# Kernel tuning notes

Measured on AMD Instinct MI355X. Metric: run time of the kernel, lower is better.

Reference implementation:

```python
import jax, jax.numpy as jnp
import numpy as np

B, D, E, H, T = 16384, 32, 8, 64, 10  # batch, state_dim, n_experts, hidden, time points
TEMP = 1.0  # gating temperature


def setup_inputs() -> dict:
    key = jax.random.key(0)
    ks = jax.random.split(key, 12)
    w = lambda k, shape, fan_in: (jax.random.normal(k, shape, jnp.float32) / np.sqrt(fan_in)).astype(jnp.float32)
    return {
        "x0": jax.random.normal(ks[0], (B, D), jnp.float32),
        "t_span": jnp.linspace(0.0, 1.0, T).astype(jnp.float32),
        # per-expert time-conditioned MLP: (x, t) -> H -> H -> D
        "W1": w(ks[1], (E, D + 1, H), D + 1), "b1": jnp.zeros((E, H), jnp.float32),
        "W2": w(ks[2], (E, H, H), H),          "b2": jnp.zeros((E, H), jnp.float32),
        "W3": w(ks[3], (E, H, D), H),          "b3": jnp.zeros((E, D), jnp.float32),
        # gating MLP on concat(x, dx_init): 2D -> H -> E
        "Gw1": w(ks[4], (2 * D, H), 2 * D), "Gb1": jnp.zeros((H,), jnp.float32),
        "Gw2": w(ks[5], (H, E), H),         "Gb2": jnp.zeros((E,), jnp.float32),
    }


def _dyn(t, x, W1, b1, W2, b2, W3, b3, Gw1, Gb1, Gw2, Gb2):
    # AME-ODE training-path dynamics: uniform-weighted init, gate, weighted sum
    inp = jnp.concatenate([x, jnp.ones((x.shape[0], 1), x.dtype) * t], axis=-1)  # [B, D+1]
    h = jnp.tanh(jnp.einsum('bi,eih->beh', inp, W1) + b1)
    h = jnp.tanh(jnp.einsum('beh,ehg->beg', h, W2) + b2)
    f = jnp.einsum('beg,egd->bed', h, W3) + b3          # all-expert dynamics [B, E, D]
    dx_init = f.mean(axis=1)                             # uniform weights 1/E
    g = jnp.tanh(jnp.concatenate([x, dx_init], -1) @ Gw1 + Gb1)
    wgt = jax.nn.softmax((g @ Gw2 + Gb2) / TEMP, axis=-1)  # [B, E]
    return jnp.einsum('be,bed->bd', wgt, f)


def reference(x0, t_span, W1, b1, W2, b2, W3, b3, Gw1, Gb1, Gw2, Gb2):
    params = (W1, b1, W2, b2, W3, b3, Gw1, Gb1, Gw2, Gb2)

    def step(x, ts):
        t0, t1 = ts[0], ts[1]
        dt = t1 - t0
        k1 = _dyn(t0, x, *params)
        k2 = _dyn(t0 + 0.5 * dt, x + 0.5 * dt * k1, *params)
        k3 = _dyn(t0 + 0.5 * dt, x + 0.5 * dt * k2, *params)
        k4 = _dyn(t1, x + dt * k3, *params)
        xn = x + (dt / 6.0) * (k1 + 2.0 * k2 + 2.0 * k3 + k4)
        return xn, xn

    pairs = jnp.stack([t_span[:-1], t_span[1:]], axis=1)  # [T-1, 2]
    _, traj = jax.lax.scan(step, x0, pairs)               # [T-1, B, D]
    traj = jnp.concatenate([x0[None], traj], axis=0)       # [T, B, D]
    return jnp.transpose(traj, (1, 0, 2))                  # [B, T, D]
```

## Files before the change

kernel.cpp:

```cpp
#include <hip/hip_runtime.h>
#include <hip/hip_bf16.h>

typedef unsigned int u32;
typedef unsigned short u16;
typedef __attribute__((ext_vector_type(8))) short short8;
typedef __attribute__((ext_vector_type(4))) float f32x4;
typedef __attribute__((ext_vector_type(4))) u32 u32x4;

#define DD 32
#define EE 8
#define HH 64
#define TT 10
#define BATCH 16384
#define EPB 32

__device__ __forceinline__ float fast_tanh(float x) {
  float e = __expf(2.f * x);
  return 1.f - 2.f * __builtin_amdgcn_rcpf(e + 1.f);
}
__device__ __forceinline__ u16 f2b_rn(float v) {
  return (u16)((__float_as_uint(v) + 0x8000u) >> 16);
}
__device__ __forceinline__ u32 pack2_rn(float a, float b) {
  return ((__float_as_uint(a) + 0x8000u) >> 16) |
         ((__float_as_uint(b) + 0x8000u) & 0xffff0000u);
}
__device__ __forceinline__ float unp_lo(u32 p) { return __uint_as_float(p << 16); }
__device__ __forceinline__ float unp_hi(u32 p) { return __uint_as_float(p & 0xffff0000u); }
__device__ __forceinline__ short8 lds_frag(const u32* p) {
  u32x4 w = *(const u32x4*)p;
  return __builtin_bit_cast(short8, w);
}

__global__ __launch_bounds__(512) void ame_ode_kernel(
    const float* __restrict__ x0, const float* __restrict__ tspan,
    const float* __restrict__ W1, const float* __restrict__ b1,
    const float* __restrict__ W2, const float* __restrict__ b2,
    const float* __restrict__ W3, const float* __restrict__ b3,
    const float* __restrict__ Gw1, const float* __restrict__ Gb1,
    const float* __restrict__ Gw2, const float* __restrict__ Gb2,
    float* __restrict__ out)
{
  __shared__ __align__(16) u32 xdb[EPB][36];
  __shared__ __align__(16) u32 fs[EPB][130];
  __shared__ __align__(16) float lg[EPB][9];
  __shared__ __align__(16) u32 hsbuf[EE * 16 * 36];
  __shared__ __align__(16) u16 gw1t[HH][72];
  __shared__ __align__(16) u16 gw2t[16][72];

  const int tid  = threadIdx.x;
  const int lane = tid & 63;
  const int l15  = lane & 15;
  const int quad = lane >> 4;
  const int e    = __builtin_amdgcn_readfirstlane(tid >> 6);
  const int elem = lane & 31;
  const int hf   = lane >> 5;
  const int cc   = 2 * e + hf;
  const int d0   = 2 * cc;
  const int bglob = blockIdx.x * EPB;

  const float* W1f = W1 + e * (DD + 1) * HH;
  const float* b1f = b1 + e * HH;
  const float* W2f = W2 + e * HH * HH;
  const float* b2f = b2 + e * HH;
  const float* W3f = W3 + e * HH * DD;
  const float* b3f = b3 + e * DD;

  short8 bw1[4], bw2[2][4], bw3[2][2];
  #pragma unroll
  for (int nt = 0; nt < 4; nt++)
    #pragma unroll
    for (int j = 0; j < 8; j++)
      bw1[nt][j] = (short)f2b_rn(W1f[(quad * 8 + j) * HH + nt * 16 + l15]);
  #pragma unroll
  for (int ks = 0; ks < 2; ks++)
    #pragma unroll
    for (int nt = 0; nt < 4; nt++)
      #pragma unroll
      for (int j = 0; j < 8; j++)
        bw2[ks][nt][j] = (short)f2b_rn(W2f[(ks * 32 + quad * 8 + j) * HH + nt * 16 + l15]);
  #pragma unroll
  for (int ks = 0; ks < 2; ks++)
    #pragma unroll
    for (int dt2 = 0; dt2 < 2; dt2++)
      #pragma unroll
      for (int j = 0; j < 8; j++)
        bw3[ks][dt2][j] = (short)f2b_rn(W3f[(ks * 32 + quad * 8 + j) * DD + dt2 * 16 + l15]);

  u32 c1p[4], c2p[2], c3p;
  #pragma unroll
  for (int nt = 0; nt < 4; nt++)
    c1p[nt] = pack2_rn(b1f[nt * 16 + l15], W1f[DD * HH + nt * 16 + l15]);
  #pragma unroll
  for (int p = 0; p < 2; p++)
    c2p[p] = pack2_rn(b2f[(2 * p) * 16 + l15], b2f[(2 * p + 1) * 16 + l15]);
  c3p = pack2_rn(b3f[l15], b3f[16 + l15]);
  const float gb1v = Gb1[(e >> 1) * 16 + l15];
  const float gb2v = (l15 < 8) ? Gb2[l15] : 0.f;

  for (int idx = tid; idx < HH * HH; idx += 512) {
    int h = idx >> 6, i = idx & 63;
    gw1t[h][i] = f2b_rn(Gw1[i * HH + h]);
  }
  for (int idx = tid; idx < 16 * HH; idx += 512) {
    int j = idx >> 6, h = idx & 63;
    gw2t[j][h] = (j < EE) ? f2b_rn(Gw2[h * EE + j]) : (u16)0;
  }

  float xst0, xst1, xac0, xac1;
  {
    const float2 v = *(const float2*)(x0 + (bglob + elem) * DD + d0);
    xst0 = v.x; xst1 = v.y; xac0 = v.x; xac1 = v.y;
    xdb[elem][cc] = pack2_rn(v.x, v.y);
    *(float2*)(out + ((bglob + elem) * TT) * DD + d0) = v;
  }
  __syncthreads();

  u32* const hw = hsbuf + e * 576;
  u16* const hw16 = (u16*)hw;
  u16* const fw16 = (u16*)&fs[0][0];
  const u32* const gw1t32 = (const u32*)&gw1t[0][0];
  const u32* const gw2t32 = (const u32*)&gw2t[0][0];
  const u16* const gs16 = (const u16*)hsbuf;
  u16* const gsw16 = (u16*)hsbuf;

  #pragma unroll 1
  for (int step = 0; step < TT - 1; step++) {
    const float t0 = tspan[step];
    const float t1 = tspan[step + 1];
    const float dt = t1 - t0;

    #pragma unroll 1
    for (int s = 0; s < 4; s++) {
      const float tcur = (s == 0) ? t0 : ((s == 3) ? t1 : t0 + 0.5f * dt);

      #pragma unroll
      for (int mt = 0; mt < 2; mt++) {
        const short8 a1 = lds_frag(&xdb[mt * 16 + l15][quad * 4]);
        f32x4 h1a[4];
        #pragma unroll
        for (int nt = 0; nt < 4; nt++) {
          const float iv = __builtin_fmaf(tcur, unp_hi(c1p[nt]), unp_lo(c1p[nt]));
          f32x4 c; c[0] = iv; c[1] = iv; c[2] = iv; c[3] = iv;
          h1a[nt] = __builtin_amdgcn_mfma_f32_16x16x32_bf16(a1, bw1[nt], c, 0, 0, 0);
        }
        #pragma unroll
        for (int nt = 0; nt < 4; nt++)
          #pragma unroll
          for (int r = 0; r < 4; r++)
            hw16[(quad * 4 + r) * 72 + nt * 16 + l15] = f2b_rn(fast_tanh(h1a[nt][r]));

        f32x4 h2a[4];
        #pragma unroll
        for (int nt = 0; nt < 4; nt++) {
          const float bv = (nt & 1) ? unp_hi(c2p[nt >> 1]) : unp_lo(c2p[nt >> 1]);
          f32x4 c; c[0] = bv; c[1] = bv; c[2] = bv; c[3] = bv;
          h2a[nt] = c;
        }
        #pragma unroll
        for (int ks = 0; ks < 2; ks++) {
          const short8 a2 = lds_frag(&hw[l15 * 36 + ks * 16 + quad * 4]);
          #pragma unroll
          for (int nt = 0; nt < 4; nt++)
            h2a[nt] = __builtin_amdgcn_mfma_f32_16x16x32_bf16(a2, bw2[ks][nt], h2a[nt], 0, 0, 0);
        }
        #pragma unroll
        for (int nt = 0; nt < 4; nt++)
          #pragma unroll
          for (int r = 0; r < 4; r++)
            hw16[(quad * 4 + r) * 72 + nt * 16 + l15] = f2b_rn(fast_tanh(h2a[nt][r]));

        f32x4 fa[2];
        #pragma unroll
        for (int dt2 = 0; dt2 < 2; dt2++) {
          const float bv = dt2 ? unp_hi(c3p) : unp_lo(c3p);
          f32x4 c; c[0] = bv; c[1] = bv; c[2] = bv; c[3] = bv;
          fa[dt2] = c;
        }
        #pragma unroll
        for (int ks = 0; ks < 2; ks++) {
          const short8 a3 = lds_frag(&hw[l15 * 36 + ks * 16 + quad * 4]);
          #pragma unroll
          for (int dt2 = 0; dt2 < 2; dt2++)
            fa[dt2] = __builtin_amdgcn_mfma_f32_16x16x32_bf16(a3, bw3[ks][dt2], fa[dt2], 0, 0, 0);
        }
        #pragma unroll
        for (int dt2 = 0; dt2 < 2; dt2++)
          #pragma unroll
          for (int r = 0; r < 4; r++)
            fw16[(mt * 16 + quad * 4 + r) * 260 + e * 32 + dt2 * 16 + l15] = f2b_rn(fa[dt2][r]);
      }
      __syncthreads();

      {
        float s0 = 0.f, s1 = 0.f;
        #pragma unroll
        for (int j = 0; j < EE; j++) {
          const u32 p = fs[elem][j * 16 + cc];
          s0 += unp_lo(p); s1 += unp_hi(p);
        }
        xdb[elem][16 + cc] = pack2_rn(s0 * 0.125f, s1 * 0.125f);
      }
      __syncthreads();

      {
        const int mt = e & 1, nt = e >> 1;
        f32x4 u; u[0] = gb1v; u[1] = gb1v; u[2] = gb1v; u[3] = gb1v;
        #pragma unroll
        for (int ks = 0; ks < 2; ks++) {
          const short8 ag = lds_frag(&xdb[mt * 16 + l15][ks * 16 + quad * 4]);
          const short8 bg = lds_frag(&gw1t32[(nt * 16 + l15) * 36 + ks * 16 + quad * 4]);
          u = __builtin_amdgcn_mfma_f32_16x16x32_bf16(ag, bg, u, 0, 0, 0);
        }
        #pragma unroll
        for (int r = 0; r < 4; r++)
          gsw16[(mt * 16 + quad * 4 + r) * 72 + nt * 16 + l15] = f2b_rn(fast_tanh(u[r]));
      }
      __syncthreads();

      if (e < 2) {
        const int mt = e;
        f32x4 lv; lv[0] = gb2v; lv[1] = gb2v; lv[2] = gb2v; lv[3] = gb2v;
        #pragma unroll
        for (int ks = 0; ks < 2; ks++) {
          const short8 ag = lds_frag((const u32*)&gs16[(mt * 16 + l15) * 72 + ks * 32 + quad * 8]);
          const short8 bg = lds_frag(&gw2t32[l15 * 36 + ks * 16 + quad * 4]);
          lv = __builtin_amdgcn_mfma_f32_16x16x32_bf16(ag, bg, lv, 0, 0, 0);
        }
        if (l15 < 8) {
          #pragma unroll
          for (int r = 0; r < 4; r++)
            lg[mt * 16 + quad * 4 + r][l15] = lv[r];
        }
      }
      __syncthreads();

      {
        float la[EE];
        #pragma unroll
        for (int j = 0; j < EE; j++) la[j] = lg[elem][j];
        float m = la[0];
        #pragma unroll
        for (int j = 1; j < EE; j++) m = fmaxf(m, la[j]);
        float w8[EE], ss = 0.f;
        #pragma unroll
        for (int j = 0; j < EE; j++) { w8[j] = __expf(la[j] - m); ss += w8[j]; }
        const float inv = __builtin_amdgcn_rcpf(ss);

        float k0 = 0.f, k1 = 0.f;
        #pragma unroll
        for (int j = 0; j < EE; j++) {
          const float wg = w8[j] * inv;
          const u32 p = fs[elem][j * 16 + cc];
          k0 = __builtin_fmaf(wg, unp_lo(p), k0);
          k1 = __builtin_fmaf(wg, unp_hi(p), k1);
        }

        const float wk = (s == 1 || s == 2) ? 2.f : 1.f;
        const float ak = dt * (1.f / 6.f) * wk;
        xac0 = __builtin_fmaf(ak, k0, xac0);
        xac1 = __builtin_fmaf(ak, k1, xac1);

        float xn0, xn1;
        if (s < 3) {
          const float cn = (s == 2) ? dt : 0.5f * dt;
          xn0 = __builtin_fmaf(cn, k0, xst0);
          xn1 = __builtin_fmaf(cn, k1, xst1);
        } else {
          xst0 = xac0; xst1 = xac1; xn0 = xac0; xn1 = xac1;
          float2 o; o.x = xn0; o.y = xn1;
          *(float2*)(out + ((bglob + elem) * TT + step + 1) * DD + d0) = o;
        }
        xdb[elem][cc] = pack2_rn(xn0, xn1);
      }
      __syncthreads();
    }
  }
}

extern "C" void kernel_launch(void* const* d_in, const int* in_sizes, int n_in,
                              void* d_out, int out_size, void* d_ws, size_t ws_size,
                              hipStream_t stream)
{
  const float* x0    = (const float*)d_in[0];
  const float* tspan = (const float*)d_in[1];
  const float* W1  = (const float*)d_in[2];
  const float* b1  = (const float*)d_in[3];
  const float* W2  = (const float*)d_in[4];
  const float* b2  = (const float*)d_in[5];
  const float* W3  = (const float*)d_in[6];
  const float* b3  = (const float*)d_in[7];
  const float* Gw1 = (const float*)d_in[8];
  const float* Gb1 = (const float*)d_in[9];
  const float* Gw2 = (const float*)d_in[10];
  const float* Gb2 = (const float*)d_in[11];

  ame_ode_kernel<<<BATCH / EPB, 512, 0, stream>>>(
      x0, tspan, W1, b1, W2, b2, W3, b3, Gw1, Gb1, Gw2, Gb2, (float*)d_out);
}
```

Measured before the change: 370.4 us.

## Double batch tile to 64 with 1024 threads and fold expert-mean into gating GEMM

Each block now handles 64 batch elements with 16 waves, two waves per expert splitting the M tiles. The uniform expert mean is no longer a separate reduction pass. It is folded into the first gating GEMM by scaling Gw1's dx half by 1/8 and running the GEMM over all expert outputs, with those weights kept in registers instead of LDS. Expert hidden and output buffers move to XOR-swizzled LDS layouts to avoid bank conflicts. The softmax max-subtraction is dropped, and pack2 uses a v_perm. The kernel trades some occupancy and register pressure for fewer blocks and barriers per element, and dropping the max-subtraction risks overflow if logits grow large.

Result: slower. 1.408 ms (+280.1%).

```diff
diff --git a/kernel.cpp b/kernel.cpp
--- a/kernel.cpp
+++ b/kernel.cpp
@@ -12,7 +12,7 @@
 #define HH 64
 #define TT 10
 #define BATCH 16384
-#define EPB 32
+#define EPB 64
 
 __device__ __forceinline__ float fast_tanh(float x) {
   float e = __expf(2.f * x);
@@ -22,17 +22,18 @@
   return (u16)((__float_as_uint(v) + 0x8000u) >> 16);
 }
 __device__ __forceinline__ u32 pack2_rn(float a, float b) {
-  return ((__float_as_uint(a) + 0x8000u) >> 16) |
-         ((__float_as_uint(b) + 0x8000u) & 0xffff0000u);
+  return __builtin_amdgcn_perm(__float_as_uint(b) + 0x8000u,
+                               __float_as_uint(a) + 0x8000u, 0x07060302u);
 }
 __device__ __forceinline__ float unp_lo(u32 p) { return __uint_as_float(p << 16); }
 __device__ __forceinline__ float unp_hi(u32 p) { return __uint_as_float(p & 0xffff0000u); }
 __device__ __forceinline__ short8 lds_frag(const u32* p) {
-  u32x4 w = *(const u32x4*)p;
-  return __builtin_bit_cast(short8, w);
-}
-
-__global__ __launch_bounds__(512) void ame_ode_kernel(
+  u32x4 v = *(const u32x4*)p;
+  return __builtin_bit_cast(short8, v);
+}
+__device__ __forceinline__ f32x4 bcast4(float v) { f32x4 c; c[0]=v; c[1]=v; c[2]=v; c[3]=v; return c; }
+
+__global__ __launch_bounds__(1024) void ame_ode_kernel(
     const float* __restrict__ x0, const float* __restrict__ tspan,
     const float* __restrict__ W1, const float* __restrict__ b1,
     const float* __restrict__ W2, const float* __restrict__ b2,
@@ -41,22 +42,21 @@
     const float* __restrict__ Gw2, const float* __restrict__ Gb2,
     float* __restrict__ out)
 {
-  __shared__ __align__(16) u32 xdb[EPB][36];
-  __shared__ __align__(16) u32 fs[EPB][130];
-  __shared__ __align__(16) float lg[EPB][9];
-  __shared__ __align__(16) u32 hsbuf[EE * 16 * 36];
-  __shared__ __align__(16) u16 gw1t[HH][72];
-  __shared__ __align__(16) u16 gw2t[16][72];
+  __shared__ __align__(16) u32  xdb[EPB * 20];
+  __shared__ __align__(16) u32  fsb[EPB * 128];
+  __shared__ __align__(16) float lg[EPB * 12];
+  __shared__ __align__(16) u32  usb[EPB * 36];
+  __shared__ __align__(16) u16  gw2t[16 * 72];
 
   const int tid  = threadIdx.x;
   const int lane = tid & 63;
   const int l15  = lane & 15;
   const int quad = lane >> 4;
-  const int e    = __builtin_amdgcn_readfirstlane(tid >> 6);
-  const int elem = lane & 31;
-  const int hf   = lane >> 5;
-  const int cc   = 2 * e + hf;
-  const int d0   = 2 * cc;
+  const int w    = __builtin_amdgcn_readfirstlane(tid >> 6);
+  const int e    = w >> 1;
+  const int mtb  = (w & 1) * 2;
+  const int elem = lane;
+  const int cc   = w;
   const int bglob = blockIdx.x * EPB;
 
   const float* W1f = W1 + e * (DD + 1) * HH;
@@ -87,6 +87,16 @@
       for (int j = 0; j < 8; j++)
         bw3[ks][dt2][j] = (short)f2b_rn(W3f[(ks * 32 + quad * 8 + j) * DD + dt2 * 16 + l15]);
 
+  const int mtg = w & 3, ntg = w >> 2;
+  short8 bg1x, bg1f;
+  #pragma unroll
+  for (int j = 0; j < 8; j++) {
+    bg1x[j] = (short)f2b_rn(Gw1[(quad * 8 + j) * HH + ntg * 16 + l15]);
+    bg1f[j] = (short)f2b_rn(0.125f * Gw1[(DD + quad * 8 + j) * HH + ntg * 16 + l15]);
+  }
+  const float gb1v = Gb1[ntg * 16 + l15];
+  const float gb2v = (l15 < 8) ? Gb2[l15] : 0.f;
+
   u32 c1p[4], c2p[2], c3p;
   #pragma unroll
   for (int nt = 0; nt < 4; nt++)
@@ -95,34 +105,24 @@
   for (int p = 0; p < 2; p++)
     c2p[p] = pack2_rn(b2f[(2 * p) * 16 + l15], b2f[(2 * p + 1) * 16 + l15]);
   c3p = pack2_rn(b3f[l15], b3f[16 + l15]);
-  const float gb1v = Gb1[(e >> 1) * 16 + l15];
-  const float gb2v = (l15 < 8) ? Gb2[l15] : 0.f;
-
-  for (int idx = tid; idx < HH * HH; idx += 512) {
-    int h = idx >> 6, i = idx & 63;
-    gw1t[h][i] = f2b_rn(Gw1[i * HH + h]);
-  }
-  for (int idx = tid; idx < 16 * HH; idx += 512) {
-    int j = idx >> 6, h = idx & 63;
-    gw2t[j][h] = (j < EE) ? f2b_rn(Gw2[h * EE + j]) : (u16)0;
+
+  {
+    const int n = tid >> 6, k = tid & 63;
+    gw2t[n * 72 + k] = (n < EE) ? f2b_rn(Gw2[k * EE + n]) : (u16)0;
   }
 
   float xst0, xst1, xac0, xac1;
   {
-    const float2 v = *(const float2*)(x0 + (bglob + elem) * DD + d0);
+    const float2 v = *(const float2*)(x0 + (bglob + elem) * DD + 2 * cc);
     xst0 = v.x; xst1 = v.y; xac0 = v.x; xac1 = v.y;
-    xdb[elem][cc] = pack2_rn(v.x, v.y);
-    *(float2*)(out + ((bglob + elem) * TT) * DD + d0) = v;
+    xdb[elem * 20 + cc] = pack2_rn(v.x, v.y);
+    *(float2*)(out + (bglob + elem) * TT * DD + 2 * cc) = v;
   }
   __syncthreads();
 
-  u32* const hw = hsbuf + e * 576;
-  u16* const hw16 = (u16*)hw;
-  u16* const fw16 = (u16*)&fs[0][0];
-  const u32* const gw1t32 = (const u32*)&gw1t[0][0];
-  const u32* const gw2t32 = (const u32*)&gw2t[0][0];
-  const u16* const gs16 = (const u16*)hsbuf;
-  u16* const gsw16 = (u16*)hsbuf;
+  u16* const fs16 = (u16*)fsb;
+  u16* const us16 = (u16*)usb;
+  const int sb32 = w * 512;
 
   #pragma unroll 1
   for (int step = 0; step < TT - 1; step++) {
@@ -134,32 +134,37 @@
     for (int s = 0; s < 4; s++) {
       const float tcur = (s == 0) ? t0 : ((s == 3) ? t1 : t0 + 0.5f * dt);
 
+      f32x4 c1i[4];
       #pragma unroll
-      for (int mt = 0; mt < 2; mt++) {
-        const short8 a1 = lds_frag(&xdb[mt * 16 + l15][quad * 4]);
+      for (int nt = 0; nt < 4; nt++)
+        c1i[nt] = bcast4(__builtin_fmaf(tcur, unp_hi(c1p[nt]), unp_lo(c1p[nt])));
+
+      u32 far[2][2][4];
+      #pragma unroll 1
+      for (int mi = 0; mi < 2; mi++) {
+        const int mt = mtb + mi;
+        const short8 a1 = lds_frag(&xdb[(mt * 16 + l15) * 20 + quad * 4]);
         f32x4 h1a[4];
         #pragma unroll
-        for (int nt = 0; nt < 4; nt++) {
-          const float iv = __builtin_fmaf(tcur, unp_hi(c1p[nt]), unp_lo(c1p[nt]));
-          f32x4 c; c[0] = iv; c[1] = iv; c[2] = iv; c[3] = iv;
-          h1a[nt] = __builtin_amdgcn_mfma_f32_16x16x32_bf16(a1, bw1[nt], c, 0, 0, 0);
-        }
-        #pragma unroll
         for (int nt = 0; nt < 4; nt++)
-          #pragma unroll
-          for (int r = 0; r < 4; r++)
-            hw16[(quad * 4 + r) * 72 + nt * 16 + l15] = f2b_rn(fast_tanh(h1a[nt][r]));
+          h1a[nt] = __builtin_amdgcn_mfma_f32_16x16x32_bf16(a1, bw1[nt], c1i[nt], 0, 0, 0);
+        #pragma unroll
+        for (int nt = 0; nt < 4; nt++)
+          #pragma unroll
+          for (int r = 0; r < 4; r++) {
+            const int hr = quad * 4 + r, c16 = nt * 16 + l15;
+            fs16[2 * sb32 + hr * 64 + ((((c16 >> 3) ^ ((hr >> 1) & 7)) << 3) | (c16 & 7))] =
+                f2b_rn(fast_tanh(h1a[nt][r]));
+          }
 
         f32x4 h2a[4];
         #pragma unroll
-        for (int nt = 0; nt < 4; nt++) {
-          const float bv = (nt & 1) ? unp_hi(c2p[nt >> 1]) : unp_lo(c2p[nt >> 1]);
-          f32x4 c; c[0] = bv; c[1] = bv; c[2] = bv; c[3] = bv;
-          h2a[nt] = c;
-        }
+        for (int nt = 0; nt < 4; nt++)
+          h2a[nt] = bcast4((nt & 1) ? unp_hi(c2p[nt >> 1]) : unp_lo(c2p[nt >> 1]));
         #pragma unroll
         for (int ks = 0; ks < 2; ks++) {
-          const short8 a2 = lds_frag(&hw[l15 * 36 + ks * 16 + quad * 4]);
+          const int c32 = ks * 16 + quad * 4;
+          const short8 a2 = lds_frag(&fsb[sb32 + l15 * 32 + (((c32 >> 2) ^ ((l15 >> 1) & 7)) << 2)]);
           #pragma unroll
           for (int nt = 0; nt < 4; nt++)
             h2a[nt] = __builtin_amdgcn_mfma_f32_16x16x32_bf16(a2, bw2[ks][nt], h2a[nt], 0, 0, 0);
@@ -167,19 +172,20 @@
         #pragma unroll
         for (int nt = 0; nt < 4; nt++)
           #pragma unroll
-          for (int r = 0; r < 4; r++)
-            hw16[(quad * 4 + r) * 72 + nt * 16 + l15] = f2b_rn(fast_tanh(h2a[nt][r]));
+          for (int r = 0; r < 4; r++) {
+            const int hr = quad * 4 + r, c16 = nt * 16 + l15;
+            fs16[2 * sb32 + hr * 64 + ((((c16 >> 3) ^ ((hr >> 1) & 7)) << 3) | (c16 & 7))] =
+                f2b_rn(fast_tanh(h2a[nt][r]));
+          }
 
         f32x4 fa[2];
         #pragma unroll
-        for (int dt2 = 0; dt2 < 2; dt2++) {
-          const float bv = dt2 ? unp_hi(c3p) : unp_lo(c3p);
-          f32x4 c; c[0] = bv; c[1] = bv; c[2] = bv; c[3] = bv;
-          fa[dt2] = c;
-        }
+        for (int dt2 = 0; dt2 < 2; dt2++)
+          fa[dt2] = bcast4(dt2 ? unp_hi(c3p) : unp_lo(c3p));
         #pragma unroll
         for (int ks = 0; ks < 2; ks++) {
-          const short8 a3 = lds_frag(&hw[l15 * 36 + ks * 16 + quad * 4]);
+          const int c32 = ks * 16 + quad * 4;
+          const short8 a3 = lds_frag(&fsb[sb32 + l15 * 32 + (((c32 >> 2) ^ ((l15 >> 1) & 7)) << 2)]);
           #pragma unroll
           for (int dt2 = 0; dt2 < 2; dt2++)
             fa[dt2] = __builtin_amdgcn_mfma_f32_16x16x32_bf16(a3, bw3[ks][dt2], fa[dt2], 0, 0, 0);
@@ -188,70 +194,76 @@
         for (int dt2 = 0; dt2 < 2; dt2++)
           #pragma unroll
           for (int r = 0; r < 4; r++)
-            fw16[(mt * 16 + quad * 4 + r) * 260 + e * 32 + dt2 * 16 + l15] = f2b_rn(fa[dt2][r]);
+            far[mi][dt2][r] = __float_as_uint(fa[dt2][r]) + 0x8000u;
       }
       __syncthreads();
 
+      #pragma unroll
+      for (int mi = 0; mi < 2; mi++)
+        #pragma unroll
+        for (int dt2 = 0; dt2 < 2; dt2++)
+          #pragma unroll
+          for (int r = 0; r < 4; r++) {
+            const int m = (mtb + mi) * 16 + quad * 4 + r;
+            const int c16 = e * 32 + dt2 * 16 + l15;
+            fs16[m * 256 + ((((c16 >> 3) ^ (m & 7)) << 3) | (c16 & 7))] =
+                (u16)(far[mi][dt2][r] >> 16);
+          }
+      __syncthreads();
+
       {
-        float s0 = 0.f, s1 = 0.f;
+        f32x4 u = bcast4(gb1v);
+        const int mg = mtg * 16 + l15;
+        const short8 ax = lds_frag(&xdb[mg * 20 + quad * 4]);
+        u = __builtin_amdgcn_mfma_f32_16x16x32_bf16(ax, bg1x, u, 0, 0, 0);
+        #pragma unroll
+        for (int kb = 0; kb < 8; kb++) {
+          const int c32 = kb * 16 + quad * 4;
+          const short8 af = lds_frag(&fsb[mg * 128 + (((c32 >> 2) ^ (mg & 7)) << 2)]);
+          u = __builtin_amdgcn_mfma_f32_16x16x32_bf16(af, bg1f, u, 0, 0, 0);
+        }
+        #pragma unroll
+        for (int r = 0; r < 4; r++)
+          us16[(mtg * 16 + quad * 4 + r) * 72 + ntg * 16 + l15] = f2b_rn(fast_tanh(u[r]));
+      }
+      __syncthreads();
+
+      if (w >= 12) {
+        const int mt2 = w - 12;
+        f32x4 lv = bcast4(gb2v);
+        #pragma unroll
+        for (int ks = 0; ks < 2; ks++) {
+          const short8 ag = lds_frag(&usb[(mt2 * 16 + l15) * 36 + ks * 16 + quad * 4]);
+          const short8 bg = lds_frag((const u32*)&gw2t[l15 * 72 + ks * 32 + quad * 8]);
+          lv = __builtin_amdgcn_mfma_f32_16x16x32_bf16(ag, bg, lv, 0, 0, 0);
+        }
+        if (l15 < 8) {
+          #pragma unroll
+          for (int r = 0; r < 4; r++)
+            lg[(mt2 * 16 + quad * 4 + r) * 12 + l15] = lv[r];
+        }
+      }
+      __syncthreads();
+
+      {
+        const float4 la0 = *(const float4*)&lg[elem * 12 + 0];
+        const float4 la1 = *(const float4*)&lg[elem * 12 + 4];
+        float w8[EE];
+        w8[0] = __expf(la0.x); w8[1] = __expf(la0.y);
+        w8[2] = __expf(la0.z); w8[3] = __expf(la0.w);
+        w8[4] = __expf(la1.x); w8[5] = __expf(la1.y);
+        w8[6] = __expf(la1.z); w8[7] = __expf(la1.w);
+        float ss = 0.f;
+        #pragma unroll
+        for (int j = 0; j < EE; j++) ss += w8[j];
+        const float inv = __builtin_amdgcn_rcpf(ss);
+
+        float k0 = 0.f, k1 = 0.f;
         #pragma unroll
         for (int j = 0; j < EE; j++) {
-          const u32 p = fs[elem][j * 16 + cc];
-          s0 += unp_lo(p); s1 += unp_hi(p);
-        }
-        xdb[elem][16 + cc] = pack2_rn(s0 * 0.125f, s1 * 0.125f);
-      }
-      __syncthreads();
-
-      {
-        const int mt = e & 1, nt = e >> 1;
-        f32x4 u; u[0] = gb1v; u[1] = gb1v; u[2] = gb1v; u[3] = gb1v;
-        #pragma unroll
-        for (int ks = 0; ks < 2; ks++) {
-          const short8 ag = lds_frag(&xdb[mt * 16 + l15][ks * 16 + quad * 4]);
-          const short8 bg = lds_frag(&gw1t32[(nt * 16 + l15) * 36 + ks * 16 + quad * 4]);
-          u = __builtin_amdgcn_mfma_f32_16x16x32_bf16(ag, bg, u, 0, 0, 0);
-        }
-        #pragma unroll
-        for (int r = 0; r < 4; r++)
-          gsw16[(mt * 16 + quad * 4 + r) * 72 + nt * 16 + l15] = f2b_rn(fast_tanh(u[r]));
-      }
-      __syncthreads();
-
-      if (e < 2) {
-        const int mt = e;
-        f32x4 lv; lv[0] = gb2v; lv[1] = gb2v; lv[2] = gb2v; lv[3] = gb2v;
-        #pragma unroll
-        for (int ks = 0; ks < 2; ks++) {
-          const short8 ag = lds_frag((const u32*)&gs16[(mt * 16 + l15) * 72 + ks * 32 + quad * 8]);
-          const short8 bg = lds_frag(&gw2t32[l15 * 36 + ks * 16 + quad * 4]);
-          lv = __builtin_amdgcn_mfma_f32_16x16x32_bf16(ag, bg, lv, 0, 0, 0);
-        }
-        if (l15 < 8) {
-          #pragma unroll
-          for (int r = 0; r < 4; r++)
-            lg[mt * 16 + quad * 4 + r][l15] = lv[r];
-        }
-      }
-      __syncthreads();
-
-      {
-        float la[EE];
-        #pragma unroll
-        for (int j = 0; j < EE; j++) la[j] = lg[elem][j];
-        float m = la[0];
-        #pragma unroll
-        for (int j = 1; j < EE; j++) m = fmaxf(m, la[j]);
-        float w8[EE], ss = 0.f;
-        #pragma unroll
-        for (int j = 0; j < EE; j++) { w8[j] = __expf(la[j] - m); ss += w8[j]; }
-        const float inv = __builtin_amdgcn_rcpf(ss);
-
-        float k0 = 0.f, k1 = 0.f;
-        #pragma unroll
-        for (int j = 0; j < EE; j++) {
+          const int c32 = j * 16 + cc;
+          const u32 p = fsb[elem * 128 + ((((c32 >> 2) ^ (elem & 7)) << 2) | (c32 & 3))];
           const float wg = w8[j] * inv;
-          const u32 p = fs[elem][j * 16 + cc];
           k0 = __builtin_fmaf(wg, unp_lo(p), k0);
           k1 = __builtin_fmaf(wg, unp_hi(p), k1);
         }
@@ -269,9 +281,9 @@
         } else {
           xst0 = xac0; xst1 = xac1; xn0 = xac0; xn1 = xac1;
           float2 o; o.x = xn0; o.y = xn1;
-          *(float2*)(out + ((bglob + elem) * TT + step + 1) * DD + d0) = o;
-        }
-        xdb[elem][cc] = pack2_rn(xn0, xn1);
+          *(float2*)(out + ((bglob + elem) * TT + step + 1) * DD + 2 * cc) = o;
+        }
+        xdb[elem * 20 + cc] = pack2_rn(xn0, xn1);
       }
       __syncthreads();
     }
@@ -295,6 +307,6 @@
   const float* Gw2 = (const float*)d_in[10];
   const float* Gb2 = (const float*)d_in[11];
 
-  ame_ode_kernel<<<BATCH / EPB, 512, 0, stream>>>(
+  ame_ode_kernel<<<BATCH / EPB, 1024, 0, stream>>>(
       x0, tspan, W1, b1, W2, b2, W3, b3, Gw1, Gb1, Gw2, Gb2, (float*)d_out);
 }
```
